# Performance work log

Measured on AMD Instinct MI355X. Metric: run time of the kernel, lower is better.

The kernel has to match this reference:

```python
import jax, jax.numpy as jnp
import numpy as np

BUCKET_SIZE = 512
# Classic perfect-spatial-hashing primes (PSH / Teschner et al.)
P1 = np.uint32(73856093)
P2 = np.uint32(19349663)
P3 = np.uint32(83492791)
P4 = np.uint32(2654435761)  # mixes batch id into the hash


def setup_inputs() -> dict:
    key = jax.random.key(0)
    k1, k2 = jax.random.split(key)
    N, B = 4_000_000, 16
    coords = jax.random.normal(k1, (N, 3), dtype=jnp.float32) * 10.0
    seps = jnp.sort(jax.random.randint(k2, (B,), 0, N, dtype=jnp.int32))
    return {"coords": coords, "seps": seps, "hash_op": 1}


def reference(coords, seps, hash_op):
    """Hash-based bucket scatter with padding (PSHScatterLayer forward).

    Each point is voxelized, spatially hashed (mixed with its batch id from
    `seps`) into one of num_buckets buckets; points are written into a padded
    [pad_to, 3] buffer at slot = bucket * BUCKET_SIZE + within-bucket rank.
    Points overflowing a bucket are dropped (finite-capacity bucket counter).
    Deterministic rank (arrival order) replaces the CUDA atomic counter.
    """
    N = coords.shape[0]
    pad_to = ((N + BUCKET_SIZE - 1) // BUCKET_SIZE) * BUCKET_SIZE
    num_buckets = pad_to // BUCKET_SIZE

    # voxelize + spatial hash (non-differentiable index path)
    vox = jnp.floor(jax.lax.stop_gradient(coords)).astype(jnp.int32).astype(jnp.uint32)  # [N,3]
    batch_id = jnp.searchsorted(seps, jnp.arange(N, dtype=seps.dtype), side='right').astype(jnp.uint32)
    h = (vox[:, 0] * P1) ^ (vox[:, 1] * P2) ^ (vox[:, 2] * P3) ^ (batch_id * P4)
    h = h + jnp.uint32(hash_op)
    bucket = (h % jnp.uint32(num_buckets)).astype(jnp.int32)  # [N]

    # per-bucket counts and within-bucket rank (stable order = arrival order)
    counts = jax.ops.segment_sum(jnp.ones((N,), jnp.int32), bucket, num_segments=num_buckets)
    starts = jnp.cumsum(counts) - counts                      # [num_buckets]
    order = jnp.argsort(bucket)                               # stable in jax
    rank_sorted = jnp.arange(N, dtype=jnp.int32) - starts[bucket[order]]
    rank = jnp.zeros((N,), jnp.int32).at[order].set(rank_sorted)

    slot = bucket * BUCKET_SIZE + rank
    idx = jnp.where(rank < BUCKET_SIZE, slot, pad_to)         # out-of-range -> dropped
    scattered_coord = jnp.zeros((pad_to, 3), coords.dtype).at[idx].set(coords, mode='drop')
    return scattered_coord, counts, bucket
```

## Files before the change

### kernel.cpp

```cpp
#include <hip/hip_runtime.h>
#include <stdint.h>

#define PR1 73856093u
#define PR2 19349663u
#define PR3 83492791u
#define PR4 2654435761u
#define GS  32
#define PPT 8
#define BBITS 13
#define SMALLB 16

__device__ __forceinline__ uint32_t fastmod(uint32_t h, uint32_t d, double inv) {
    uint32_t q = (uint32_t)((double)h * inv);
    int32_t r = (int32_t)(h - q * d);
    if (r >= (int32_t)d) r -= d;
    if (r < 0) r += d;
    return (uint32_t)r;
}

__device__ __forceinline__ int chunk_of(int bi, int C) {
    return ((C & 7) == 0) ? ((bi & 7) * (C >> 3) + (bi >> 3)) : bi;
}

__device__ __forceinline__ uint32_t bucket_of(float x, float y, float z,
                                              uint32_t bid, uint32_t hop,
                                              uint32_t NBu, double invNB) {
    const uint32_t vx = (uint32_t)(int32_t)floorf(x);
    const uint32_t vy = (uint32_t)(int32_t)floorf(y);
    const uint32_t vz = (uint32_t)(int32_t)floorf(z);
    uint32_t h = vx * PR1 ^ vy * PR2 ^ vz * PR3 ^ (bid * PR4);
    h += hop;
    return fastmod(h, NBu, invNB);
}

__global__ __launch_bounds__(256)
void k_bucket_hist(const float* __restrict__ coords,
                   const int* __restrict__ seps, int B,
                   const int* __restrict__ hash_op_p,
                   int N, int NB, int C, int chunk, double invNB,
                   float* __restrict__ out_bucket,
                   uint16_t* __restrict__ ch) {
    extern __shared__ int hist[];
    __shared__ int s_seps[1024];
    const int tid = threadIdx.x;
    for (int i = tid; i < NB; i += blockDim.x) hist[i] = 0;
    const bool smallB = (B <= SMALLB);
    int sv[SMALLB];
    if (smallB) {
        #pragma unroll
        for (int j = 0; j < SMALLB; j++) sv[j] = (j < B) ? seps[j] : 0x7fffffff;
    } else {
        const int Bc = B < 1024 ? B : 1024;
        for (int j = tid; j < Bc; j += blockDim.x) s_seps[j] = seps[j];
    }
    __syncthreads();

    const uint32_t hop = (uint32_t)hash_op_p[0];
    const uint32_t NBu = (uint32_t)NB;
    const int c = chunk_of(blockIdx.x, C);
    const int start = c * chunk;
    const int end   = min(start + chunk, N);
    int bid = 0;
    for (int i0 = start + tid * 4; i0 < end; i0 += (int)blockDim.x * 4) {
        const int navail = end - i0;
        float xs[4], ys[4], zs[4];
        if (navail >= 4) {
            const float4* cp = (const float4*)(coords + 3 * (size_t)i0);
            const float4 a = cp[0], b4 = cp[1], c4 = cp[2];
            xs[0] = a.x;  ys[0] = a.y;  zs[0] = a.z;
            xs[1] = a.w;  ys[1] = b4.x; zs[1] = b4.y;
            xs[2] = b4.z; ys[2] = b4.w; zs[2] = c4.x;
            xs[3] = c4.y; ys[3] = c4.z; zs[3] = c4.w;
        } else {
            #pragma unroll
            for (int p = 0; p < 4; p++) {
                const int i = i0 + p;
                if (i < end) {
                    xs[p] = coords[3 * (size_t)i + 0];
                    ys[p] = coords[3 * (size_t)i + 1];
                    zs[p] = coords[3 * (size_t)i + 2];
                } else { xs[p] = ys[p] = zs[p] = 0.f; }
            }
        }
        float bf[4];
        #pragma unroll
        for (int p = 0; p < 4; p++) {
            const int i = i0 + p;
            if (i < end) {
                int mybid;
                if (smallB) {
                    mybid = 0;
                    #pragma unroll
                    for (int j = 0; j < SMALLB; j++) mybid += (sv[j] <= i) ? 1 : 0;
                } else {
                    while (bid < B) {
                        const int svv = (bid < 1024) ? s_seps[bid] : seps[bid];
                        if (svv <= i) bid++; else break;
                    }
                    mybid = bid;
                }
                const uint32_t b = bucket_of(xs[p], ys[p], zs[p],
                                             (uint32_t)mybid, hop, NBu, invNB);
                bf[p] = (float)b;
                atomicAdd(&hist[(int)b], 1);
            } else bf[p] = 0.f;
        }
        if (navail >= 4) {
            *(float4*)(out_bucket + i0) = make_float4(bf[0], bf[1], bf[2], bf[3]);
        } else {
            for (int p = 0; p < navail; p++) out_bucket[i0 + p] = bf[p];
        }
    }
    __syncthreads();
    uint16_t* dst = ch + (size_t)c * NB;
    for (int i = tid; i < NB; i += blockDim.x) dst[i] = (uint16_t)hist[i];
}

__global__ void k_scan_group(uint16_t* __restrict__ ch, int* __restrict__ Sg,
                             int C, int NB) {
    const int b = blockIdx.x * blockDim.x + threadIdx.x;
    if (b >= NB) return;
    const int g  = blockIdx.y;
    const int c0 = g * GS;
    const int c1 = min(c0 + GS, C);
    int run = 0;
    for (int c = c0; c < c1; c++) {
        const size_t idx = (size_t)c * NB + b;
        const int v = ch[idx];
        ch[idx] = (uint16_t)(run < 512 ? run : 512);
        run += v;
    }
    Sg[(size_t)g * NB + b] = run;
}

__global__ void k_scan_tops(int* __restrict__ Sg, int G, int NB,
                            float* __restrict__ out_counts,
                            float* __restrict__ out_sc) {
    const int b = blockIdx.x * blockDim.x + threadIdx.x;
    if (b >= NB) return;
    int run = 0;
    for (int g = 0; g < G; g++) {
        const size_t idx = (size_t)g * NB + b;
        const int v = Sg[idx];
        Sg[idx] = run;
        run += v;
    }
    out_counts[b] = (float)run;
    const int c0 = run < 512 ? run : 512;
    float* p = out_sc + ((size_t)b * 512 + c0) * 3;
    for (int j = c0; j < 512; j++) {
        p[0] = 0.f; p[1] = 0.f; p[2] = 0.f;
        p += 3;
    }
}

__global__ __launch_bounds__(256, 4)
void k_scatter(const float* __restrict__ coords,
               const int* __restrict__ seps, int B,
               const int* __restrict__ hash_op_p,
               const uint16_t* __restrict__ ch,
               const int* __restrict__ Sg,
               int N, int NB, int C, int chunk, double invNB,
               float* __restrict__ out_sc) {
    extern __shared__ int hist[];
    const int tid = threadIdx.x;
    const int c = chunk_of(blockIdx.x, C);
    const int g = c / GS;
    const uint16_t* r1 = ch + (size_t)c * NB;
    const int*      r2 = Sg + (size_t)g * NB;
    for (int i = tid; i < NB; i += blockDim.x) hist[i] = (int)r1[i] + r2[i];
    __syncthreads();

    const bool smallB = (B <= SMALLB);
    int sv[SMALLB];
    if (smallB) {
        #pragma unroll
        for (int j = 0; j < SMALLB; j++) sv[j] = (j < B) ? seps[j] : 0x7fffffff;
    }
    const uint32_t hop = (uint32_t)hash_op_p[0];
    const uint32_t NBu = (uint32_t)NB;

    const int start = c * chunk;
    const int end   = min(start + chunk, N);
    const int len   = end > start ? end - start : 0;
    const int per_round = (int)blockDim.x * PPT;
    const int rounds = (len + per_round - 1) / per_round;
    const int lane = tid & 63;
    const int wv   = tid >> 6;
    const int nw   = (int)blockDim.x >> 6;
    const unsigned long long ltmask = ((unsigned long long)1 << lane) - 1;
    int fb_bid = 0;

    for (int rd = 0; rd < rounds; rd++) {
        const int wbase = start + rd * per_round + wv * (64 * PPT);
        int bs[PPT], leader[PPT], cntv[PPT], rnk[PPT];
        float cx[PPT], cy[PPT], cz[PPT];

        #pragma unroll
        for (int s = 0; s < PPT; s++) {
            const int i = wbase + s * 64 + lane;
            const bool v = (i < end);
            cx[s] = v ? coords[3 * (size_t)i + 0] : 0.f;
            cy[s] = v ? coords[3 * (size_t)i + 1] : 0.f;
            cz[s] = v ? coords[3 * (size_t)i + 2] : 0.f;
            if (v) {
                int mybid;
                if (smallB) {
                    mybid = 0;
                    #pragma unroll
                    for (int j = 0; j < SMALLB; j++) mybid += (sv[j] <= i) ? 1 : 0;
                } else {
                    while (fb_bid < B) {
                        if (seps[fb_bid] <= i) fb_bid++; else break;
                    }
                    mybid = fb_bid;
                }
                bs[s] = (int)bucket_of(cx[s], cy[s], cz[s],
                                       (uint32_t)mybid, hop, NBu, invNB);
            } else {
                bs[s] = NB;
            }
        }

        #pragma unroll
        for (int s = 0; s < PPT; s++) {
            const int b = bs[s];
            unsigned long long mm = ~0ull;
            #pragma unroll
            for (int k = 0; k < BBITS; k++) {
                const unsigned long long blt = __ballot(((b >> k) & 1) != 0);
                mm &= ((b >> k) & 1) ? blt : ~blt;
            }
            leader[s] = (int)__builtin_ctzll(mm);
            cntv[s]   = (int)__builtin_popcountll(mm);
            rnk[s]    = (int)__builtin_popcountll(mm & ltmask);
        }

        int basev[PPT];
        for (int w = 0; w < nw; w++) {
            if (wv == w) {
                #pragma unroll
                for (int s = 0; s < PPT; s++) {
                    int old = 0;
                    if (bs[s] < NB && lane == leader[s])
                        old = atomicAdd(&hist[bs[s]], cntv[s]);
                    basev[s] = __shfl(old, leader[s], 64);
                }
            }
            __syncthreads();
        }

        #pragma unroll
        for (int s = 0; s < PPT; s++) {
            if (bs[s] < NB) {
                const int r = basev[s] + rnk[s];
                if (r < 512) {
                    float* p = out_sc + ((size_t)bs[s] * 512 + r) * 3;
                    p[0] = cx[s]; p[1] = cy[s]; p[2] = cz[s];
                }
            }
        }
    }
}

extern "C" void kernel_launch(void* const* d_in, const int* in_sizes, int n_in,
                              void* d_out, int out_size, void* d_ws, size_t ws_size,
                              hipStream_t stream) {
    const float* coords  = (const float*)d_in[0];
    const int*   seps    = (const int*)d_in[1];
    const int*   hash_op = (const int*)d_in[2];

    const int N = in_sizes[0] / 3;
    const int B = in_sizes[1];
    const int pad_to = ((N + 511) / 512) * 512;
    const int NB = pad_to / 512;

    float* out        = (float*)d_out;
    float* out_counts = out + (size_t)pad_to * 3;
    float* out_bucket = out_counts + NB;

    int C = 1024;
    while (C > 8) {
        const int G_ = (C + GS - 1) / GS;
        if ((size_t)C * NB * 2 + (size_t)G_ * NB * 4 <= ws_size) break;
        C -= 8;
    }
    const int G = (C + GS - 1) / GS;
    int chunk = (N + C - 1) / C;
    chunk = (chunk + 3) & ~3;
    uint16_t* ch = (uint16_t*)d_ws;
    int* Sg = (int*)((char*)d_ws + (((size_t)C * NB * 2 + 15) & ~(size_t)15));
    const size_t lds = (size_t)NB * sizeof(int);
    const double invNB = 1.0 / (double)NB;

    k_bucket_hist<<<C, 256, lds, stream>>>(coords, seps, B, hash_op, N, NB, C,
                                           chunk, invNB, out_bucket, ch);
    dim3 g2a((NB + 63) / 64, G);
    k_scan_group<<<g2a, 64, 0, stream>>>(ch, Sg, C, NB);
    k_scan_tops<<<(NB + 63) / 64, 64, 0, stream>>>(Sg, G, NB, out_counts, out);
    k_scatter<<<C, 256, lds, stream>>>(coords, seps, B, hash_op, ch, Sg,
                                       N, NB, C, chunk, invNB, out);
}
```

Measured before the change: 199.1 us.

## Use single-wavefront scatter blocks to drop serialized per-wave barriers

The scatter kernel now runs one 64-lane wavefront per block instead of four, which removes the loop that serialized waves with __syncthreads to keep ranks in arrival order. Each round's ballot-based match, the leader's LDS atomic, the broadcast and the store now happen inline per slot, so fewer per-slot arrays stay live in registers. The cost is that each block has a quarter of the threads, so the per-chunk histogram init and the point loop get less parallelism. Occupancy now depends on how many LDS-heavy blocks fit per CU.

```diff
diff --git a/kernel.cpp b/kernel.cpp
--- a/kernel.cpp
+++ b/kernel.cpp
@@ -154,7 +154,7 @@
     }
 }
 
-__global__ __launch_bounds__(256, 4)
+__global__ __launch_bounds__(64)
 void k_scatter(const float* __restrict__ coords,
                const int* __restrict__ seps, int B,
                const int* __restrict__ hash_op_p,
@@ -163,12 +163,12 @@
                int N, int NB, int C, int chunk, double invNB,
                float* __restrict__ out_sc) {
     extern __shared__ int hist[];
-    const int tid = threadIdx.x;
+    const int lane = threadIdx.x;
     const int c = chunk_of(blockIdx.x, C);
     const int g = c / GS;
     const uint16_t* r1 = ch + (size_t)c * NB;
     const int*      r2 = Sg + (size_t)g * NB;
-    for (int i = tid; i < NB; i += blockDim.x) hist[i] = (int)r1[i] + r2[i];
+    for (int i = lane; i < NB; i += 64) hist[i] = (int)r1[i] + r2[i];
     __syncthreads();
 
     const bool smallB = (B <= SMALLB);
@@ -183,27 +183,29 @@
     const int start = c * chunk;
     const int end   = min(start + chunk, N);
     const int len   = end > start ? end - start : 0;
-    const int per_round = (int)blockDim.x * PPT;
+    const int per_round = 64 * PPT;
     const int rounds = (len + per_round - 1) / per_round;
-    const int lane = tid & 63;
-    const int wv   = tid >> 6;
-    const int nw   = (int)blockDim.x >> 6;
     const unsigned long long ltmask = ((unsigned long long)1 << lane) - 1;
     int fb_bid = 0;
 
     for (int rd = 0; rd < rounds; rd++) {
-        const int wbase = start + rd * per_round + wv * (64 * PPT);
-        int bs[PPT], leader[PPT], cntv[PPT], rnk[PPT];
+        const int base = start + rd * per_round;
         float cx[PPT], cy[PPT], cz[PPT];
 
         #pragma unroll
         for (int s = 0; s < PPT; s++) {
-            const int i = wbase + s * 64 + lane;
+            const int i = base + s * 64 + lane;
             const bool v = (i < end);
             cx[s] = v ? coords[3 * (size_t)i + 0] : 0.f;
             cy[s] = v ? coords[3 * (size_t)i + 1] : 0.f;
             cz[s] = v ? coords[3 * (size_t)i + 2] : 0.f;
-            if (v) {
+        }
+
+        int bs[PPT];
+        #pragma unroll
+        for (int s = 0; s < PPT; s++) {
+            const int i = base + s * 64 + lane;
+            if (i < end) {
                 int mybid;
                 if (smallB) {
                     mybid = 0;
@@ -231,31 +233,17 @@
                 const unsigned long long blt = __ballot(((b >> k) & 1) != 0);
                 mm &= ((b >> k) & 1) ? blt : ~blt;
             }
-            leader[s] = (int)__builtin_ctzll(mm);
-            cntv[s]   = (int)__builtin_popcountll(mm);
-            rnk[s]    = (int)__builtin_popcountll(mm & ltmask);
-        }
-
-        int basev[PPT];
-        for (int w = 0; w < nw; w++) {
-            if (wv == w) {
-                #pragma unroll
-                for (int s = 0; s < PPT; s++) {
-                    int old = 0;
-                    if (bs[s] < NB && lane == leader[s])
-                        old = atomicAdd(&hist[bs[s]], cntv[s]);
-                    basev[s] = __shfl(old, leader[s], 64);
-                }
-            }
-            __syncthreads();
-        }
-
-        #pragma unroll
-        for (int s = 0; s < PPT; s++) {
-            if (bs[s] < NB) {
-                const int r = basev[s] + rnk[s];
+            const int leader = (int)__builtin_ctzll(mm);
+            const int cnt    = (int)__builtin_popcountll(mm);
+            const int rnk    = (int)__builtin_popcountll(mm & ltmask);
+            int old = 0;
+            if (b < NB && lane == leader)
+                old = atomicAdd(&hist[b], cnt);
+            const int bbase = __shfl(old, leader, 64);
+            if (b < NB) {
+                const int r = bbase + rnk;
                 if (r < 512) {
-                    float* p = out_sc + ((size_t)bs[s] * 512 + r) * 3;
+                    float* p = out_sc + ((size_t)b * 512 + r) * 3;
                     p[0] = cx[s]; p[1] = cy[s]; p[2] = cz[s];
                 }
             }
@@ -298,6 +286,6 @@
     dim3 g2a((NB + 63) / 64, G);
     k_scan_group<<<g2a, 64, 0, stream>>>(ch, Sg, C, NB);
     k_scan_tops<<<(NB + 63) / 64, 64, 0, stream>>>(Sg, G, NB, out_counts, out);
-    k_scatter<<<C, 256, lds, stream>>>(coords, seps, B, hash_op, ch, Sg,
-                                       N, NB, C, chunk, invNB, out);
-}
+    k_scatter<<<C, 64, lds, stream>>>(coords, seps, B, hash_op, ch, Sg,
+                                      N, NB, C, chunk, invNB, out);
+}
```

After: 217.5 us. +9.3%, slower.

## Pack per-block bucket histograms into 16-bit LDS halves and double chunk count

Applied to the files above, without the earlier changes.

Shared-memory histograms in both the histogram and scatter kernels now hold two 16-bit bucket counters per 32-bit word, halving LDS per block. Scatter offsets are clamped to 512 so they cannot overflow into the neighbouring half. The chunk count is raised from 1024 to 2048 to use the extra occupancy. This relies on per-chunk counts fitting in 16 bits, and the extra chunks add scan work and workspace.

```diff
diff --git a/kernel.cpp b/kernel.cpp
--- a/kernel.cpp
+++ b/kernel.cpp
@@ -40,10 +40,11 @@
                    int N, int NB, int C, int chunk, double invNB,
                    float* __restrict__ out_bucket,
                    uint16_t* __restrict__ ch) {
-    extern __shared__ int hist[];
+    extern __shared__ unsigned int histp[];
     __shared__ int s_seps[1024];
     const int tid = threadIdx.x;
-    for (int i = tid; i < NB; i += blockDim.x) hist[i] = 0;
+    const int half = (NB + 1) >> 1;
+    for (int i = tid; i < half; i += blockDim.x) histp[i] = 0u;
     const bool smallB = (B <= SMALLB);
     int sv[SMALLB];
     if (smallB) {
@@ -99,10 +100,10 @@
                     }
                     mybid = bid;
                 }
-                const uint32_t b = bucket_of(xs[p], ys[p], zs[p],
+                const int b = (int)bucket_of(xs[p], ys[p], zs[p],
                                              (uint32_t)mybid, hop, NBu, invNB);
                 bf[p] = (float)b;
-                atomicAdd(&hist[(int)b], 1);
+                atomicAdd(&histp[b >> 1], 1u << ((b & 1) * 16));
             } else bf[p] = 0.f;
         }
         if (navail >= 4) {
@@ -113,7 +114,8 @@
     }
     __syncthreads();
     uint16_t* dst = ch + (size_t)c * NB;
-    for (int i = tid; i < NB; i += blockDim.x) dst[i] = (uint16_t)hist[i];
+    for (int i = tid; i < NB; i += blockDim.x)
+        dst[i] = (uint16_t)((histp[i >> 1] >> ((i & 1) * 16)) & 0xffffu);
 }
 
 __global__ void k_scan_group(uint16_t* __restrict__ ch, int* __restrict__ Sg,
@@ -162,13 +164,20 @@
                const int* __restrict__ Sg,
                int N, int NB, int C, int chunk, double invNB,
                float* __restrict__ out_sc) {
-    extern __shared__ int hist[];
+    extern __shared__ unsigned int histp[];
     const int tid = threadIdx.x;
     const int c = chunk_of(blockIdx.x, C);
     const int g = c / GS;
     const uint16_t* r1 = ch + (size_t)c * NB;
     const int*      r2 = Sg + (size_t)g * NB;
-    for (int i = tid; i < NB; i += blockDim.x) hist[i] = (int)r1[i] + r2[i];
+    const int half = (NB + 1) >> 1;
+    for (int i = tid; i < half; i += blockDim.x) {
+        const int b0 = 2 * i, b1 = 2 * i + 1;
+        int v0 = (int)r1[b0] + r2[b0]; v0 = v0 < 512 ? v0 : 512;
+        int v1 = 512;
+        if (b1 < NB) { v1 = (int)r1[b1] + r2[b1]; v1 = v1 < 512 ? v1 : 512; }
+        histp[i] = (unsigned)v0 | ((unsigned)v1 << 16);
+    }
     __syncthreads();
 
     const bool smallB = (B <= SMALLB);
@@ -242,8 +251,13 @@
                 #pragma unroll
                 for (int s = 0; s < PPT; s++) {
                     int old = 0;
-                    if (bs[s] < NB && lane == leader[s])
-                        old = atomicAdd(&hist[bs[s]], cntv[s]);
+                    const int b = bs[s];
+                    if (b < NB && lane == leader[s]) {
+                        const unsigned oldp =
+                            atomicAdd(&histp[b >> 1],
+                                      (unsigned)cntv[s] << ((b & 1) * 16));
+                        old = (int)((oldp >> ((b & 1) * 16)) & 0xffffu);
+                    }
                     basev[s] = __shfl(old, leader[s], 64);
                 }
             }
@@ -279,10 +293,10 @@
     float* out_counts = out + (size_t)pad_to * 3;
     float* out_bucket = out_counts + NB;
 
-    int C = 1024;
+    int C = 2048;
     while (C > 8) {
         const int G_ = (C + GS - 1) / GS;
-        if ((size_t)C * NB * 2 + (size_t)G_ * NB * 4 <= ws_size) break;
+        if ((size_t)C * NB * 2 + (size_t)G_ * NB * 4 + 64 <= ws_size) break;
         C -= 8;
     }
     const int G = (C + GS - 1) / GS;
@@ -290,7 +304,7 @@
     chunk = (chunk + 3) & ~3;
     uint16_t* ch = (uint16_t*)d_ws;
     int* Sg = (int*)((char*)d_ws + (((size_t)C * NB * 2 + 15) & ~(size_t)15));
-    const size_t lds = (size_t)NB * sizeof(int);
+    const size_t lds = ((size_t)(NB + 1) / 2) * sizeof(unsigned int);
     const double invNB = 1.0 / (double)NB;
 
     k_bucket_hist<<<C, 256, lds, stream>>>(coords, seps, B, hash_op, N, NB, C,
```

New measurement: 216.7 us. 1.09x slower.

## Compute within-chunk ranks in histogram pass and reuse them in scatter

Applied to the files above, without the earlier changes.

The ballot-based ranking moves from the scatter kernel into the first histogram kernel, which now writes a per-point 16-bit local rank to workspace. The scatter kernel no longer rehashes or reranks. It reads the stored bucket and rank, adds the chunk's base offset from LDS, and writes coordinates with vectorized loads. This removes the duplicated hash and ballot work in the second pass. In exchange it adds an extra N*2-byte rank array to write and read back, and the first kernel now uses uncoalesced strided coordinate loads and per-round barriers.

```diff
diff --git a/kernel.cpp b/kernel.cpp
--- a/kernel.cpp
+++ b/kernel.cpp
@@ -33,12 +33,13 @@
     return fastmod(h, NBu, invNB);
 }
 
-__global__ __launch_bounds__(256)
-void k_bucket_hist(const float* __restrict__ coords,
+__global__ __launch_bounds__(256, 4)
+void k_bucket_rank(const float* __restrict__ coords,
                    const int* __restrict__ seps, int B,
                    const int* __restrict__ hash_op_p,
                    int N, int NB, int C, int chunk, double invNB,
                    float* __restrict__ out_bucket,
+                   uint16_t* __restrict__ rank_out,
                    uint16_t* __restrict__ ch) {
     extern __shared__ int hist[];
     __shared__ int s_seps[1024];
@@ -60,58 +61,80 @@
     const int c = chunk_of(blockIdx.x, C);
     const int start = c * chunk;
     const int end   = min(start + chunk, N);
-    int bid = 0;
-    for (int i0 = start + tid * 4; i0 < end; i0 += (int)blockDim.x * 4) {
-        const int navail = end - i0;
-        float xs[4], ys[4], zs[4];
-        if (navail >= 4) {
-            const float4* cp = (const float4*)(coords + 3 * (size_t)i0);
-            const float4 a = cp[0], b4 = cp[1], c4 = cp[2];
-            xs[0] = a.x;  ys[0] = a.y;  zs[0] = a.z;
-            xs[1] = a.w;  ys[1] = b4.x; zs[1] = b4.y;
-            xs[2] = b4.z; ys[2] = b4.w; zs[2] = c4.x;
-            xs[3] = c4.y; ys[3] = c4.z; zs[3] = c4.w;
-        } else {
-            #pragma unroll
-            for (int p = 0; p < 4; p++) {
-                const int i = i0 + p;
-                if (i < end) {
-                    xs[p] = coords[3 * (size_t)i + 0];
-                    ys[p] = coords[3 * (size_t)i + 1];
-                    zs[p] = coords[3 * (size_t)i + 2];
-                } else { xs[p] = ys[p] = zs[p] = 0.f; }
-            }
-        }
-        float bf[4];
-        #pragma unroll
-        for (int p = 0; p < 4; p++) {
-            const int i = i0 + p;
+    const int len   = end > start ? end - start : 0;
+    const int per_round = (int)blockDim.x * PPT;
+    const int rounds = (len + per_round - 1) / per_round;
+    const int lane = tid & 63;
+    const int wv   = tid >> 6;
+    const int nw   = (int)blockDim.x >> 6;
+    const unsigned long long ltmask = ((unsigned long long)1 << lane) - 1;
+    int fb_bid = 0;
+
+    for (int rd = 0; rd < rounds; rd++) {
+        const int wbase = start + rd * per_round + wv * (64 * PPT);
+        int bs[PPT], leader[PPT], cntv[PPT], rnk[PPT];
+
+        #pragma unroll
+        for (int s = 0; s < PPT; s++) {
+            const int i = wbase + s * 64 + lane;
             if (i < end) {
+                const float x = coords[3 * (size_t)i + 0];
+                const float y = coords[3 * (size_t)i + 1];
+                const float z = coords[3 * (size_t)i + 2];
                 int mybid;
                 if (smallB) {
                     mybid = 0;
                     #pragma unroll
                     for (int j = 0; j < SMALLB; j++) mybid += (sv[j] <= i) ? 1 : 0;
                 } else {
-                    while (bid < B) {
-                        const int svv = (bid < 1024) ? s_seps[bid] : seps[bid];
-                        if (svv <= i) bid++; else break;
+                    while (fb_bid < B) {
+                        if (seps[fb_bid] <= i) fb_bid++; else break;
                     }
-                    mybid = bid;
-                }
-                const uint32_t b = bucket_of(xs[p], ys[p], zs[p],
-                                             (uint32_t)mybid, hop, NBu, invNB);
-                bf[p] = (float)b;
-                atomicAdd(&hist[(int)b], 1);
-            } else bf[p] = 0.f;
-        }
-        if (navail >= 4) {
-            *(float4*)(out_bucket + i0) = make_float4(bf[0], bf[1], bf[2], bf[3]);
-        } else {
-            for (int p = 0; p < navail; p++) out_bucket[i0 + p] = bf[p];
-        }
-    }
-    __syncthreads();
+                    mybid = fb_bid;
+                }
+                bs[s] = (int)bucket_of(x, y, z, (uint32_t)mybid, hop, NBu, invNB);
+            } else {
+                bs[s] = NB;
+            }
+        }
+
+        #pragma unroll
+        for (int s = 0; s < PPT; s++) {
+            const int b = bs[s];
+            unsigned long long mm = ~0ull;
+            #pragma unroll
+            for (int k = 0; k < BBITS; k++) {
+                const unsigned long long blt = __ballot(((b >> k) & 1) != 0);
+                mm &= ((b >> k) & 1) ? blt : ~blt;
+            }
+            leader[s] = (int)__builtin_ctzll(mm);
+            cntv[s]   = (int)__builtin_popcountll(mm);
+            rnk[s]    = (int)__builtin_popcountll(mm & ltmask);
+        }
+
+        int basev[PPT];
+        for (int w = 0; w < nw; w++) {
+            if (wv == w) {
+                #pragma unroll
+                for (int s = 0; s < PPT; s++) {
+                    int old = 0;
+                    if (bs[s] < NB && lane == leader[s])
+                        old = atomicAdd(&hist[bs[s]], cntv[s]);
+                    basev[s] = __shfl(old, leader[s], 64);
+                }
+            }
+            __syncthreads();
+        }
+
+        #pragma unroll
+        for (int s = 0; s < PPT; s++) {
+            const int i = wbase + s * 64 + lane;
+            if (i < end) {
+                out_bucket[i] = (float)bs[s];
+                rank_out[i] = (uint16_t)(basev[s] + rnk[s]);
+            }
+        }
+    }
     uint16_t* dst = ch + (size_t)c * NB;
     for (int i = tid; i < NB; i += blockDim.x) dst[i] = (uint16_t)hist[i];
 }
@@ -154,109 +177,62 @@
     }
 }
 
-__global__ __launch_bounds__(256, 4)
+__global__ __launch_bounds__(256)
 void k_scatter(const float* __restrict__ coords,
-               const int* __restrict__ seps, int B,
-               const int* __restrict__ hash_op_p,
+               const float* __restrict__ bucket_f,
+               const uint16_t* __restrict__ rank_in,
                const uint16_t* __restrict__ ch,
                const int* __restrict__ Sg,
-               int N, int NB, int C, int chunk, double invNB,
+               int N, int NB, int C, int chunk,
                float* __restrict__ out_sc) {
-    extern __shared__ int hist[];
+    extern __shared__ uint16_t base16[];
     const int tid = threadIdx.x;
     const int c = chunk_of(blockIdx.x, C);
     const int g = c / GS;
     const uint16_t* r1 = ch + (size_t)c * NB;
     const int*      r2 = Sg + (size_t)g * NB;
-    for (int i = tid; i < NB; i += blockDim.x) hist[i] = (int)r1[i] + r2[i];
+    for (int i = tid; i < NB; i += blockDim.x) {
+        const int v = (int)r1[i] + r2[i];
+        base16[i] = (uint16_t)(v < 512 ? v : 512);
+    }
     __syncthreads();
-
-    const bool smallB = (B <= SMALLB);
-    int sv[SMALLB];
-    if (smallB) {
-        #pragma unroll
-        for (int j = 0; j < SMALLB; j++) sv[j] = (j < B) ? seps[j] : 0x7fffffff;
-    }
-    const uint32_t hop = (uint32_t)hash_op_p[0];
-    const uint32_t NBu = (uint32_t)NB;
 
     const int start = c * chunk;
     const int end   = min(start + chunk, N);
-    const int len   = end > start ? end - start : 0;
-    const int per_round = (int)blockDim.x * PPT;
-    const int rounds = (len + per_round - 1) / per_round;
-    const int lane = tid & 63;
-    const int wv   = tid >> 6;
-    const int nw   = (int)blockDim.x >> 6;
-    const unsigned long long ltmask = ((unsigned long long)1 << lane) - 1;
-    int fb_bid = 0;
-
-    for (int rd = 0; rd < rounds; rd++) {
-        const int wbase = start + rd * per_round + wv * (64 * PPT);
-        int bs[PPT], leader[PPT], cntv[PPT], rnk[PPT];
-        float cx[PPT], cy[PPT], cz[PPT];
-
-        #pragma unroll
-        for (int s = 0; s < PPT; s++) {
-            const int i = wbase + s * 64 + lane;
-            const bool v = (i < end);
-            cx[s] = v ? coords[3 * (size_t)i + 0] : 0.f;
-            cy[s] = v ? coords[3 * (size_t)i + 1] : 0.f;
-            cz[s] = v ? coords[3 * (size_t)i + 2] : 0.f;
-            if (v) {
-                int mybid;
-                if (smallB) {
-                    mybid = 0;
-                    #pragma unroll
-                    for (int j = 0; j < SMALLB; j++) mybid += (sv[j] <= i) ? 1 : 0;
-                } else {
-                    while (fb_bid < B) {
-                        if (seps[fb_bid] <= i) fb_bid++; else break;
-                    }
-                    mybid = fb_bid;
-                }
-                bs[s] = (int)bucket_of(cx[s], cy[s], cz[s],
-                                       (uint32_t)mybid, hop, NBu, invNB);
-            } else {
-                bs[s] = NB;
-            }
-        }
-
-        #pragma unroll
-        for (int s = 0; s < PPT; s++) {
-            const int b = bs[s];
-            unsigned long long mm = ~0ull;
+    for (int i0 = start + tid * 4; i0 < end; i0 += (int)blockDim.x * 4) {
+        const int navail = end - i0;
+        if (navail >= 4) {
+            const float4* cp = (const float4*)(coords + 3 * (size_t)i0);
+            const float4 a = cp[0], b4 = cp[1], c4 = cp[2];
+            float xs[4], ys[4], zs[4];
+            xs[0] = a.x;  ys[0] = a.y;  zs[0] = a.z;
+            xs[1] = a.w;  ys[1] = b4.x; zs[1] = b4.y;
+            xs[2] = b4.z; ys[2] = b4.w; zs[2] = c4.x;
+            xs[3] = c4.y; ys[3] = c4.z; zs[3] = c4.w;
+            const float4 bf4 = *(const float4*)(bucket_f + i0);
+            const ushort4 rr = *(const ushort4*)(rank_in + i0);
+            int bk[4], rk[4];
+            bk[0] = (int)bf4.x; bk[1] = (int)bf4.y;
+            bk[2] = (int)bf4.z; bk[3] = (int)bf4.w;
+            rk[0] = rr.x; rk[1] = rr.y; rk[2] = rr.z; rk[3] = rr.w;
             #pragma unroll
-            for (int k = 0; k < BBITS; k++) {
-                const unsigned long long blt = __ballot(((b >> k) & 1) != 0);
-                mm &= ((b >> k) & 1) ? blt : ~blt;
-            }
-            leader[s] = (int)__builtin_ctzll(mm);
-            cntv[s]   = (int)__builtin_popcountll(mm);
-            rnk[s]    = (int)__builtin_popcountll(mm & ltmask);
-        }
-
-        int basev[PPT];
-        for (int w = 0; w < nw; w++) {
-            if (wv == w) {
-                #pragma unroll
-                for (int s = 0; s < PPT; s++) {
-                    int old = 0;
-                    if (bs[s] < NB && lane == leader[s])
-                        old = atomicAdd(&hist[bs[s]], cntv[s]);
-                    basev[s] = __shfl(old, leader[s], 64);
-                }
-            }
-            __syncthreads();
-        }
-
-        #pragma unroll
-        for (int s = 0; s < PPT; s++) {
-            if (bs[s] < NB) {
-                const int r = basev[s] + rnk[s];
+            for (int p = 0; p < 4; p++) {
+                const int r = (int)base16[bk[p]] + rk[p];
                 if (r < 512) {
-                    float* p = out_sc + ((size_t)bs[s] * 512 + r) * 3;
-                    p[0] = cx[s]; p[1] = cy[s]; p[2] = cz[s];
+                    float* q = out_sc + ((size_t)bk[p] * 512 + r) * 3;
+                    q[0] = xs[p]; q[1] = ys[p]; q[2] = zs[p];
+                }
+            }
+        } else {
+            for (int p = 0; p < navail; p++) {
+                const int i = i0 + p;
+                const int b = (int)bucket_f[i];
+                const int r = (int)base16[b] + rank_in[i];
+                if (r < 512) {
+                    float* q = out_sc + ((size_t)b * 512 + r) * 3;
+                    q[0] = coords[3 * (size_t)i + 0];
+                    q[1] = coords[3 * (size_t)i + 1];
+                    q[2] = coords[3 * (size_t)i + 2];
                 }
             }
         }
@@ -279,25 +255,31 @@
     float* out_counts = out + (size_t)pad_to * 3;
     float* out_bucket = out_counts + NB;
 
+    const size_t rank_bytes = (size_t)N * 2;
     int C = 1024;
     while (C > 8) {
         const int G_ = (C + GS - 1) / GS;
-        if ((size_t)C * NB * 2 + (size_t)G_ * NB * 4 <= ws_size) break;
+        if ((size_t)C * NB * 2 + (size_t)G_ * NB * 4 + rank_bytes + 64
+            <= ws_size) break;
         C -= 8;
     }
     const int G = (C + GS - 1) / GS;
     int chunk = (N + C - 1) / C;
     chunk = (chunk + 3) & ~3;
     uint16_t* ch = (uint16_t*)d_ws;
-    int* Sg = (int*)((char*)d_ws + (((size_t)C * NB * 2 + 15) & ~(size_t)15));
-    const size_t lds = (size_t)NB * sizeof(int);
+    size_t off = ((size_t)C * NB * 2 + 15) & ~(size_t)15;
+    int* Sg = (int*)((char*)d_ws + off);
+    off = (off + (size_t)G * NB * 4 + 15) & ~(size_t)15;
+    uint16_t* rank_ws = (uint16_t*)((char*)d_ws + off);
+    const size_t lds1 = (size_t)NB * sizeof(int);
+    const size_t lds3 = (size_t)NB * sizeof(uint16_t);
     const double invNB = 1.0 / (double)NB;
 
-    k_bucket_hist<<<C, 256, lds, stream>>>(coords, seps, B, hash_op, N, NB, C,
-                                           chunk, invNB, out_bucket, ch);
+    k_bucket_rank<<<C, 256, lds1, stream>>>(coords, seps, B, hash_op, N, NB, C,
+                                            chunk, invNB, out_bucket, rank_ws, ch);
     dim3 g2a((NB + 63) / 64, G);
     k_scan_group<<<g2a, 64, 0, stream>>>(ch, Sg, C, NB);
     k_scan_tops<<<(NB + 63) / 64, 64, 0, stream>>>(Sg, G, NB, out_counts, out);
-    k_scatter<<<C, 256, lds, stream>>>(coords, seps, B, hash_op, ch, Sg,
-                                       N, NB, C, chunk, invNB, out);
-}
+    k_scatter<<<C, 256, lds3, stream>>>(coords, out_bucket, rank_ws, ch, Sg,
+                                        N, NB, C, chunk, out);
+}
```

After: 227.8 us. 1.14x slower.
